# Performance work log

Hardware: AMD Instinct MI355X
Metric: run time of the kernel (lower is better)

The kernel has to match this reference:

```python
import jax, jax.numpy as jnp
import numpy as np

N = 100000   # nodes
E = 640000   # edges
D = 128      # feature dim
G = 512      # graphs in the batch


def setup_inputs() -> dict:
    key = jax.random.key(0)
    ks = jax.random.split(key, 6)
    x = jax.random.normal(ks[0], (N, D), dtype=jnp.float32)
    edge_index = jax.random.randint(ks[1], (2, E), 0, N, dtype=jnp.int32)
    batch = jnp.sort(jax.random.randint(ks[2], (N,), 0, G, dtype=jnp.int32))
    scale = 1.0 / np.sqrt(D)
    W0 = jax.random.normal(ks[3], (D, D), dtype=jnp.float32) * scale
    W1 = jax.random.normal(ks[4], (D, D), dtype=jnp.float32) * scale
    W2 = jax.random.normal(ks[5], (D, D), dtype=jnp.float32) * scale
    return {"x": x, "edge_index": edge_index, "batch": batch,
            "W0": W0, "W1": W1, "W2": W2}


def gcn_conv(x, W, row, col, n):
    """GCNConv (bias=False): x' = D^-1/2 (A + I) D^-1/2 (x @ W).
    row/col already include self-loops."""
    xw = x @ W                                              # [N, D]
    deg = jax.ops.segment_sum(jnp.ones_like(col, dtype=x.dtype), col,
                              num_segments=n)               # [N]
    dinv = jnp.where(deg > 0, jax.lax.rsqrt(deg), 0.0)
    norm = dinv[row] * dinv[col]                            # [E+N]
    msgs = norm[:, None] * xw[row]                          # gather + scale
    return jax.ops.segment_sum(msgs, col, num_segments=n)   # scatter-add


def reference(x, edge_index, batch, W0, W1, W2):
    n = x.shape[0]
    loops = jnp.arange(n, dtype=edge_index.dtype)
    row = jnp.concatenate([edge_index[0], loops])
    col = jnp.concatenate([edge_index[1], loops])
    # conv_layers[:-1] (no activation between them in forward)
    x = gcn_conv(x, W0, row, col, n)
    x = gcn_conv(x, W1, row, col, n)
    x = jax.nn.leaky_relu(x, negative_slope=0.01)
    x = gcn_conv(x, W2, row, col, n)
    # global_add_pool over graph ids
    return jax.ops.segment_sum(x, batch, num_segments=G)    # [G, D]
```

## Files before the change

kernel.cpp:

```cpp
#include <hip/hip_runtime.h>
#include <hip/hip_bf16.h>

#define FEAT 128

typedef unsigned int uint32;
typedef unsigned long long uint64;
typedef unsigned short ushort16;
typedef __attribute__((ext_vector_type(8))) short short8;
typedef __attribute__((ext_vector_type(4))) float v4f;
typedef __attribute__((ext_vector_type(2))) float f32x2;

__device__ __forceinline__ ushort16 f2bf(float f) {
    uint32 u = __float_as_uint(f);
    u += 0x7fffu + ((u >> 16) & 1u);
    return (ushort16)(u >> 16);
}
__device__ __forceinline__ float bflo(uint32 u) { return __uint_as_float(u << 16); }
__device__ __forceinline__ float bfhi(uint32 u) { return __uint_as_float(u & 0xffff0000u); }
__device__ __forceinline__ f32x2 up2(uint32 u) { return (f32x2){bflo(u), bfhi(u)}; }

__global__ __launch_bounds__(256) void hydra_kernel(const float* __restrict__ x,
                                                    ushort16* __restrict__ Xh,
                                                    const int* __restrict__ col,
                                                    int* __restrict__ counts,
                                                    const float* __restrict__ W0,
                                                    const float* __restrict__ W1,
                                                    ushort16* __restrict__ W01t,
                                                    float* __restrict__ Pbuf,
                                                    int cvtBlocks, int histBlocks,
                                                    int total8, int E) {
    int b = blockIdx.x;
    int t = threadIdx.x;
    if (b < cvtBlocks) {
        int id = b * 256 + t;
        if (id < total8) {
            const float4 v0 = *(const float4*)(x + (size_t)id * 8);
            const float4 v1 = *(const float4*)(x + (size_t)id * 8 + 4);
            uint4 o;
            o.x = (uint32)f2bf(v0.x) | ((uint32)f2bf(v0.y) << 16);
            o.y = (uint32)f2bf(v0.z) | ((uint32)f2bf(v0.w) << 16);
            o.z = (uint32)f2bf(v1.x) | ((uint32)f2bf(v1.y) << 16);
            o.w = (uint32)f2bf(v1.z) | ((uint32)f2bf(v1.w) << 16);
            *(uint4*)(Xh + (size_t)id * 8) = o;
        }
    } else if (b < cvtBlocks + histBlocks) {
        int id = (b - cvtBlocks) * 256 + t;
        if (id * 4 + 3 < E) {
            int4 c4 = *(const int4*)(col + id * 4);
            atomicAdd(&counts[c4.x], 1);
            atomicAdd(&counts[c4.y], 1);
            atomicAdd(&counts[c4.z], 1);
            atomicAdd(&counts[c4.w], 1);
        } else {
            for (int e = id * 4; e < E; e++) atomicAdd(&counts[col[e]], 1);
        }
    } else if (b < cvtBlocks + histBlocks + 64) {
        __shared__ float sW0[2][FEAT];
        int wb = b - cvtBlocks - histBlocks;
        int lk = t >> 7;
        int ncol = t & 127;
        int k = wb * 2 + lk;
        sW0[lk][ncol] = W0[(size_t)k * FEAT + ncol];
        __syncthreads();
        float acc = 0.f;
#pragma unroll 4
        for (int j = 0; j < FEAT; j++)
            acc += sW0[lk][j] * W1[(size_t)j * FEAT + ncol];
        W01t[(size_t)ncol * FEAT + k] = f2bf(acc);
    } else {
        int zb = b - cvtBlocks - histBlocks - 64;
        float4 z = make_float4(0.f, 0.f, 0.f, 0.f);
        float* p = Pbuf + (size_t)zb * 2048 + t * 8;
        *(float4*)p = z;
        *(float4*)(p + 4) = z;
    }
}

__global__ __launch_bounds__(256) void scan_part(const int* __restrict__ counts,
                                                 int* __restrict__ bsum, int n) {
    __shared__ int s[256];
    int base = blockIdx.x * 1024;
    int t = threadIdx.x;
    int v = 0;
#pragma unroll
    for (int i = 0; i < 4; i++) {
        int idx = base + t * 4 + i;
        if (idx < n) v += counts[idx];
    }
    s[t] = v;
    __syncthreads();
    for (int o = 128; o > 0; o >>= 1) {
        if (t < o) s[t] += s[t + o];
        __syncthreads();
    }
    if (t == 0) bsum[blockIdx.x] = s[0];
}

__global__ __launch_bounds__(256) void scan_final(const int* __restrict__ counts,
                                                  const int* __restrict__ bsum,
                                                  int* __restrict__ off, int* __restrict__ nxt,
                                                  float* __restrict__ dinv, int n, int nb) {
    __shared__ int s[256];
    __shared__ int sb[128];
    int base = blockIdx.x * 1024;
    int t = threadIdx.x;
    if (t < nb) sb[t] = bsum[t];
    int c[4];
    int sum = 0;
#pragma unroll
    for (int i = 0; i < 4; i++) {
        int idx = base + t * 4 + i;
        c[i] = (idx < n) ? counts[idx] : 0;
        sum += c[i];
    }
    int v0 = sum;
    s[t] = sum;
    __syncthreads();
    for (int o = 1; o < 256; o <<= 1) {
        int v = (t >= o) ? s[t - o] : 0;
        __syncthreads();
        s[t] += v;
        __syncthreads();
    }
    int blockBase = 0;
    for (int j = 0; j < blockIdx.x; j++) blockBase += sb[j];
    int excl = s[t] - v0 + blockBase;
#pragma unroll
    for (int i = 0; i < 4; i++) {
        int idx = base + t * 4 + i;
        if (idx < n) {
            off[idx] = excl;
            nxt[idx] = excl;
            dinv[idx] = rsqrtf((float)(c[i] + 1));
        }
        excl += c[i];
    }
    if (blockIdx.x == gridDim.x - 1 && t == 255) off[n] = excl;
}

__global__ void fill_kernel(const int* __restrict__ row, const int* __restrict__ col,
                            int* __restrict__ nxt,
                            int* __restrict__ srcArr, int E) {
    int e = blockIdx.x * 256 + threadIdx.x;
    if (e < E) {
        int c = col[e], r = row[e];
        int p = atomicAdd(&nxt[c], 1);
        __builtin_nontemporal_store(r, &srcArr[p]);
    }
}

__global__ __launch_bounds__(256) void gemm_mfma(const ushort16* __restrict__ A,
                                                 const ushort16* __restrict__ Wt,
                                                 ushort16* __restrict__ Ch, int n,
                                                 int leaky) {
    const int t = threadIdx.x;
    const int w = t >> 6;
    const int lane = t & 63;
    const int quad = lane >> 4;
    const int l16 = lane & 15;
    const int colBase = (w & 1) * 64;

    short8 wf[4][4];
#pragma unroll
    for (int ct = 0; ct < 4; ct++) {
        const ushort16* wp = Wt + (size_t)(colBase + ct * 16 + l16) * FEAT + quad * 8;
#pragma unroll
        for (int ks = 0; ks < 4; ks++) wf[ct][ks] = *(const short8*)(wp + ks * 32);
    }

    const int nTiles = (n + 15) >> 4;
    const int tStride = gridDim.x * 2;
    int tile = blockIdx.x * 2 + (w >> 1);
    if (tile >= nTiles) return;

    auto loadA = [&](int tl, short8 (&a)[4]) {
        const int row = tl * 16 + l16;
        if (row < n) {
            const ushort16* ap = A + (size_t)row * FEAT + quad * 8;
#pragma unroll
            for (int ks = 0; ks < 4; ks++) a[ks] = *(const short8*)(ap + ks * 32);
        } else {
#pragma unroll
            for (int ks = 0; ks < 4; ks++) a[ks] = (short8)0;
        }
    };

    short8 aCur[4];
    loadA(tile, aCur);

    while (tile < nTiles) {
        const int nextTile = tile + tStride;
        short8 aNxt[4];
        if (nextTile < nTiles) loadA(nextTile, aNxt);

        v4f acc[4];
#pragma unroll
        for (int ct = 0; ct < 4; ct++) acc[ct] = (v4f)0.f;
#pragma unroll
        for (int ct = 0; ct < 4; ct++)
#pragma unroll
            for (int ks = 0; ks < 4; ks++)
                acc[ct] = __builtin_amdgcn_mfma_f32_16x16x32_bf16(wf[ct][ks], aCur[ks], acc[ct], 0, 0, 0);

        const int row = tile * 16 + l16;
        if (row < n) {
#pragma unroll
            for (int ct = 0; ct < 4; ct++) {
                float p0 = acc[ct][0], p1 = acc[ct][1], p2 = acc[ct][2], p3 = acc[ct][3];
                if (leaky) {
                    p0 = (p0 >= 0.f) ? p0 : 0.01f * p0;
                    p1 = (p1 >= 0.f) ? p1 : 0.01f * p1;
                    p2 = (p2 >= 0.f) ? p2 : 0.01f * p2;
                    p3 = (p3 >= 0.f) ? p3 : 0.01f * p3;
                }
                uint2 o;
                o.x = (uint32)f2bf(p0) | ((uint32)f2bf(p1) << 16);
                o.y = (uint32)f2bf(p2) | ((uint32)f2bf(p3) << 16);
                *(uint2*)(Ch + (size_t)row * FEAT + colBase + ct * 16 + quad * 4) = o;
            }
        }

        tile = nextTile;
#pragma unroll
        for (int ks = 0; ks < 4; ks++) aCur[ks] = aNxt[ks];
    }
}

__global__ __launch_bounds__(256) void gather_kernel(const int* __restrict__ off,
                                                     const int* __restrict__ srcArr,
                                                     const float* __restrict__ dinv,
                                                     const ushort16* __restrict__ XWh,
                                                     ushort16* __restrict__ Hh, int n) {
    int node = blockIdx.x * 4 + (threadIdx.x >> 6);
    if (node >= n) return;
    int lane = threadIdx.x & 63;
    int grp = lane >> 4;
    int l16 = lane & 15;
    float dc = dinv[node];
    const uint4* table = (const uint4*)XWh;

    f32x2 acc[4];
    if (grp == 0) {
        uint4 v = table[(size_t)node * 16 + l16];
        f32x2 w0 = (f32x2){dc * dc, dc * dc};
        acc[0] = w0 * up2(v.x);
        acc[1] = w0 * up2(v.y);
        acc[2] = w0 * up2(v.z);
        acc[3] = w0 * up2(v.w);
    } else {
#pragma unroll
        for (int j = 0; j < 4; j++) acc[j] = (f32x2){0.f, 0.f};
    }

    int s = off[node], e = off[node + 1];
    int i = s + grp;
    for (; i + 4 < e; i += 8) {
        int r0 = srcArr[i];
        int r1 = srcArr[i + 4];
        uint4 u0 = table[(size_t)r0 * 16 + l16];
        uint4 u1 = table[(size_t)r1 * 16 + l16];
        float f0 = dc * dinv[r0];
        float f1 = dc * dinv[r1];
        f32x2 n0 = (f32x2){f0, f0};
        f32x2 n1 = (f32x2){f1, f1};
        acc[0] += n0 * up2(u0.x);
        acc[1] += n0 * up2(u0.y);
        acc[2] += n0 * up2(u0.z);
        acc[3] += n0 * up2(u0.w);
        acc[0] += n1 * up2(u1.x);
        acc[1] += n1 * up2(u1.y);
        acc[2] += n1 * up2(u1.z);
        acc[3] += n1 * up2(u1.w);
    }
    if (i < e) {
        int r0 = srcArr[i];
        uint4 u0 = table[(size_t)r0 * 16 + l16];
        float f0 = dc * dinv[r0];
        f32x2 n0 = (f32x2){f0, f0};
        acc[0] += n0 * up2(u0.x);
        acc[1] += n0 * up2(u0.y);
        acc[2] += n0 * up2(u0.z);
        acc[3] += n0 * up2(u0.w);
    }

    float b[8] = {acc[0].x, acc[0].y, acc[1].x, acc[1].y,
                  acc[2].x, acc[2].y, acc[3].x, acc[3].y};
#pragma unroll
    for (int j = 0; j < 8; j++) {
        b[j] += __shfl_xor(b[j], 16);
        b[j] += __shfl_xor(b[j], 32);
    }

    if (grp == 0) {
        uint4 o;
        o.x = (uint32)f2bf(b[0]) | ((uint32)f2bf(b[1]) << 16);
        o.y = (uint32)f2bf(b[2]) | ((uint32)f2bf(b[3]) << 16);
        o.z = (uint32)f2bf(b[4]) | ((uint32)f2bf(b[5]) << 16);
        o.w = (uint32)f2bf(b[6]) | ((uint32)f2bf(b[7]) << 16);
        *(uint4*)(Hh + (size_t)node * FEAT + l16 * 8) = o;
    }
}

__global__ __launch_bounds__(128) void pool_kernel(const ushort16* __restrict__ H,
                                                   const int* __restrict__ batch,
                                                   float* __restrict__ P, int n) {
    int t = threadIdx.x;
    int i0 = blockIdx.x * 64;
    if (i0 >= n) return;
    int i1 = min(i0 + 64, n);
    float acc = 0.f;
    int g = batch[i0];
    for (int i = i0; i < i1; i++) {
        int b = batch[i];
        if (b != g) {
            atomicAdd(&P[(size_t)g * FEAT + t], acc);
            acc = 0.f;
            g = b;
        }
        uint32 u = (uint32)(unsigned short)H[(size_t)i * FEAT + t];
        acc += __uint_as_float(u << 16);
    }
    atomicAdd(&P[(size_t)g * FEAT + t], acc);
}

__global__ __launch_bounds__(128) void pgemm_kernel(const float* __restrict__ P,
                                                    const float* __restrict__ W2,
                                                    float* __restrict__ out) {
    __shared__ float sP[FEAT];
    const int g = blockIdx.x;
    const int t = threadIdx.x;
    sP[t] = P[(size_t)g * FEAT + t];
    __syncthreads();
    float o = 0.f;
#pragma unroll 4
    for (int k = 0; k < FEAT; k++) o += sP[k] * W2[(size_t)k * FEAT + t];
    out[(size_t)g * FEAT + t] = o;
}

extern "C" void kernel_launch(void* const* d_in, const int* in_sizes, int n_in,
                              void* d_out, int out_size, void* d_ws, size_t ws_size,
                              hipStream_t stream) {
    const float* x = (const float*)d_in[0];
    const int* ei = (const int*)d_in[1];
    const int* batch = (const int*)d_in[2];
    const float* W0 = (const float*)d_in[3];
    const float* W1 = (const float*)d_in[4];
    const float* W2 = (const float*)d_in[5];
    float* out = (float*)d_out;

    const int N = in_sizes[0] / FEAT;
    const int E = in_sizes[1] / 2;
    const int G = out_size / FEAT;

    const int* rowI = ei;
    const int* colI = ei + E;

    char* ws = (char*)d_ws;
    auto take = [&](size_t bytes) {
        char* p = ws;
        ws += (bytes + 15) & ~(size_t)15;
        return p;
    };
    int* counts    = (int*)take((size_t)N * 4);
    int* off       = (int*)take((size_t)(N + 1) * 4);
    int* nxt       = (int*)take((size_t)N * 4);
    float* dinv    = (float*)take((size_t)N * 4);
    int* bsum      = (int*)take(128 * 4);
    int* srcArr    = (int*)take((size_t)E * 4);
    ushort16* W01t = (ushort16*)take((size_t)16384 * 2);
    float* Pbuf    = (float*)take((size_t)G * FEAT * 4);
    ushort16* Xh   = (ushort16*)take((size_t)N * FEAT * 2);
    ushort16* bufA = (ushort16*)take((size_t)N * FEAT * 2);
    ushort16* bufB = (ushort16*)take((size_t)N * FEAT * 2);

    const int nb = (N + 1023) / 1024;
    const int eb = (E + 255) / 256;

    hipMemsetAsync(counts, 0, (size_t)N * 4, stream);
    const int total8 = N * FEAT / 8;
    const int cvtBlocks = (total8 + 255) / 256;
    const int histBlocks = (E + 1023) / 1024;
    hydra_kernel<<<cvtBlocks + histBlocks + 64 + 32, 256, 0, stream>>>(
        x, Xh, colI, counts, W0, W1, W01t, Pbuf, cvtBlocks, histBlocks, total8, E);

    scan_part<<<nb, 256, 0, stream>>>(counts, bsum, N);
    scan_final<<<nb, 256, 0, stream>>>(counts, bsum, off, nxt, dinv, N, nb);
    fill_kernel<<<eb, 256, 0, stream>>>(rowI, colI, nxt, srcArr, E);

    const int gatBlocks = (N + 3) / 4;

    gather_kernel<<<gatBlocks, 256, 0, stream>>>(off, srcArr, dinv, Xh, bufA, N);
    gather_kernel<<<gatBlocks, 256, 0, stream>>>(off, srcArr, dinv, bufA, bufB, N);
    gemm_mfma<<<1024, 256, 0, stream>>>(bufB, W01t, bufA, N, 1);
    gather_kernel<<<gatBlocks, 256, 0, stream>>>(off, srcArr, dinv, bufA, bufB, N);
    pool_kernel<<<(N + 63) / 64, 128, 0, stream>>>(bufB, batch, Pbuf, N);
    pgemm_kernel<<<G, 128, 0, stream>>>(Pbuf, W2, out);
}
```

Baseline: 361.1 us.

## Apply fused weight GEMM before propagation and fuse leaky ReLU into gather

Reorders the two linear GCN layers so the combined W0·W1 GEMM runs first, reading fp32 x directly and converting to bf16 in registers. This drops the separate x-to-bf16 conversion pass and its intermediate buffer. The leaky ReLU moves from the GEMM epilogue into the second gather's output stage. Rounding order changes slightly, since the projected features are quantized before aggregation.

Result: no change. 365.2 us (+1.1%).

```diff
diff --git a/kernel.cpp b/kernel.cpp
--- a/kernel.cpp
+++ b/kernel.cpp
@@ -1,10 +1,10 @@
 #include <hip/hip_runtime.h>
 #include <hip/hip_bf16.h>
+#include <type_traits>
 
 #define FEAT 128
 
 typedef unsigned int uint32;
-typedef unsigned long long uint64;
 typedef unsigned short ushort16;
 typedef __attribute__((ext_vector_type(8))) short short8;
 typedef __attribute__((ext_vector_type(4))) float v4f;
@@ -19,32 +19,17 @@
 __device__ __forceinline__ float bfhi(uint32 u) { return __uint_as_float(u & 0xffff0000u); }
 __device__ __forceinline__ f32x2 up2(uint32 u) { return (f32x2){bflo(u), bfhi(u)}; }
 
-__global__ __launch_bounds__(256) void hydra_kernel(const float* __restrict__ x,
-                                                    ushort16* __restrict__ Xh,
-                                                    const int* __restrict__ col,
+__global__ __launch_bounds__(256) void hydra_kernel(const int* __restrict__ col,
                                                     int* __restrict__ counts,
                                                     const float* __restrict__ W0,
                                                     const float* __restrict__ W1,
                                                     ushort16* __restrict__ W01t,
                                                     float* __restrict__ Pbuf,
-                                                    int cvtBlocks, int histBlocks,
-                                                    int total8, int E) {
+                                                    int histBlocks, int E) {
     int b = blockIdx.x;
     int t = threadIdx.x;
-    if (b < cvtBlocks) {
+    if (b < histBlocks) {
         int id = b * 256 + t;
-        if (id < total8) {
-            const float4 v0 = *(const float4*)(x + (size_t)id * 8);
-            const float4 v1 = *(const float4*)(x + (size_t)id * 8 + 4);
-            uint4 o;
-            o.x = (uint32)f2bf(v0.x) | ((uint32)f2bf(v0.y) << 16);
-            o.y = (uint32)f2bf(v0.z) | ((uint32)f2bf(v0.w) << 16);
-            o.z = (uint32)f2bf(v1.x) | ((uint32)f2bf(v1.y) << 16);
-            o.w = (uint32)f2bf(v1.z) | ((uint32)f2bf(v1.w) << 16);
-            *(uint4*)(Xh + (size_t)id * 8) = o;
-        }
-    } else if (b < cvtBlocks + histBlocks) {
-        int id = (b - cvtBlocks) * 256 + t;
         if (id * 4 + 3 < E) {
             int4 c4 = *(const int4*)(col + id * 4);
             atomicAdd(&counts[c4.x], 1);
@@ -54,9 +39,9 @@
         } else {
             for (int e = id * 4; e < E; e++) atomicAdd(&counts[col[e]], 1);
         }
-    } else if (b < cvtBlocks + histBlocks + 64) {
+    } else if (b < histBlocks + 64) {
         __shared__ float sW0[2][FEAT];
-        int wb = b - cvtBlocks - histBlocks;
+        int wb = b - histBlocks;
         int lk = t >> 7;
         int ncol = t & 127;
         int k = wb * 2 + lk;
@@ -68,7 +53,7 @@
             acc += sW0[lk][j] * W1[(size_t)j * FEAT + ncol];
         W01t[(size_t)ncol * FEAT + k] = f2bf(acc);
     } else {
-        int zb = b - cvtBlocks - histBlocks - 64;
+        int zb = b - histBlocks - 64;
         float4 z = make_float4(0.f, 0.f, 0.f, 0.f);
         float* p = Pbuf + (size_t)zb * 2048 + t * 8;
         *(float4*)p = z;
@@ -149,7 +134,8 @@
     }
 }
 
-__global__ __launch_bounds__(256) void gemm_mfma(const ushort16* __restrict__ A,
+template <typename T>
+__global__ __launch_bounds__(256) void gemm_mfma(const T* __restrict__ A,
                                                  const ushort16* __restrict__ Wt,
                                                  ushort16* __restrict__ Ch, int n,
                                                  int leaky) {
@@ -176,9 +162,22 @@
     auto loadA = [&](int tl, short8 (&a)[4]) {
         const int row = tl * 16 + l16;
         if (row < n) {
-            const ushort16* ap = A + (size_t)row * FEAT + quad * 8;
-#pragma unroll
-            for (int ks = 0; ks < 4; ks++) a[ks] = *(const short8*)(ap + ks * 32);
+            if constexpr (std::is_same<T, float>::value) {
+#pragma unroll
+                for (int ks = 0; ks < 4; ks++) {
+                    const float* ap = A + (size_t)row * FEAT + quad * 8 + ks * 32;
+                    float4 f0 = *(const float4*)ap;
+                    float4 f1 = *(const float4*)(ap + 4);
+                    short8 v;
+                    v[0] = f2bf(f0.x); v[1] = f2bf(f0.y); v[2] = f2bf(f0.z); v[3] = f2bf(f0.w);
+                    v[4] = f2bf(f1.x); v[5] = f2bf(f1.y); v[6] = f2bf(f1.z); v[7] = f2bf(f1.w);
+                    a[ks] = v;
+                }
+            } else {
+                const ushort16* ap = A + (size_t)row * FEAT + quad * 8;
+#pragma unroll
+                for (int ks = 0; ks < 4; ks++) a[ks] = *(const short8*)(ap + ks * 32);
+            }
         } else {
 #pragma unroll
             for (int ks = 0; ks < 4; ks++) a[ks] = (short8)0;
@@ -230,7 +229,8 @@
                                                      const int* __restrict__ srcArr,
                                                      const float* __restrict__ dinv,
                                                      const ushort16* __restrict__ XWh,
-                                                     ushort16* __restrict__ Hh, int n) {
+                                                     ushort16* __restrict__ Hh, int n,
+                                                     int leaky) {
     int node = blockIdx.x * 4 + (threadIdx.x >> 6);
     if (node >= n) return;
     int lane = threadIdx.x & 63;
@@ -292,6 +292,10 @@
     }
 
     if (grp == 0) {
+        if (leaky) {
+#pragma unroll
+            for (int j = 0; j < 8; j++) b[j] = (b[j] >= 0.f) ? b[j] : 0.01f * b[j];
+        }
         uint4 o;
         o.x = (uint32)f2bf(b[0]) | ((uint32)f2bf(b[1]) << 16);
         o.y = (uint32)f2bf(b[2]) | ((uint32)f2bf(b[3]) << 16);
@@ -369,7 +373,6 @@
     int* srcArr    = (int*)take((size_t)E * 4);
     ushort16* W01t = (ushort16*)take((size_t)16384 * 2);
     float* Pbuf    = (float*)take((size_t)G * FEAT * 4);
-    ushort16* Xh   = (ushort16*)take((size_t)N * FEAT * 2);
     ushort16* bufA = (ushort16*)take((size_t)N * FEAT * 2);
     ushort16* bufB = (ushort16*)take((size_t)N * FEAT * 2);
 
@@ -377,11 +380,9 @@
     const int eb = (E + 255) / 256;
 
     hipMemsetAsync(counts, 0, (size_t)N * 4, stream);
-    const int total8 = N * FEAT / 8;
-    const int cvtBlocks = (total8 + 255) / 256;
     const int histBlocks = (E + 1023) / 1024;
-    hydra_kernel<<<cvtBlocks + histBlocks + 64 + 32, 256, 0, stream>>>(
-        x, Xh, colI, counts, W0, W1, W01t, Pbuf, cvtBlocks, histBlocks, total8, E);
+    hydra_kernel<<<histBlocks + 64 + 32, 256, 0, stream>>>(
+        colI, counts, W0, W1, W01t, Pbuf, histBlocks, E);
 
     scan_part<<<nb, 256, 0, stream>>>(counts, bsum, N);
     scan_final<<<nb, 256, 0, stream>>>(counts, bsum, off, nxt, dinv, N, nb);
@@ -389,10 +390,10 @@
 
     const int gatBlocks = (N + 3) / 4;
 
-    gather_kernel<<<gatBlocks, 256, 0, stream>>>(off, srcArr, dinv, Xh, bufA, N);
-    gather_kernel<<<gatBlocks, 256, 0, stream>>>(off, srcArr, dinv, bufA, bufB, N);
-    gemm_mfma<<<1024, 256, 0, stream>>>(bufB, W01t, bufA, N, 1);
-    gather_kernel<<<gatBlocks, 256, 0, stream>>>(off, srcArr, dinv, bufA, bufB, N);
+    gemm_mfma<float><<<1024, 256, 0, stream>>>(x, W01t, bufA, N, 0);
+    gather_kernel<<<gatBlocks, 256, 0, stream>>>(off, srcArr, dinv, bufA, bufB, N, 0);
+    gather_kernel<<<gatBlocks, 256, 0, stream>>>(off, srcArr, dinv, bufB, bufA, N, 1);
+    gather_kernel<<<gatBlocks, 256, 0, stream>>>(off, srcArr, dinv, bufA, bufB, N, 0);
     pool_kernel<<<(N + 63) / 64, 128, 0, stream>>>(bufB, batch, Pbuf, N);
     pgemm_kernel<<<G, 128, 0, stream>>>(Pbuf, W2, out);
 }
```
